# Optimization experiments

Measured on AMD Instinct MI355X. Metric: run time of the kernel, lower is better.

## Reference

```python
import jax, jax.numpy as jnp
import numpy as np

B, T, D = 4, 4096, 1024
EPS = 1e-5


def _layernorm(x, w):
    mu = jnp.mean(x, axis=-1, keepdims=True)
    var = jnp.var(x, axis=-1, keepdims=True)
    return (x - mu) * jax.lax.rsqrt(var + EPS) * w


def setup_inputs() -> dict:
    key = jax.random.key(0)
    k0, k1, k2, k3 = jax.random.split(key, 4)
    x = jax.random.normal(k0, (B, T, D), dtype=jnp.float32)
    lengths = jax.random.randint(k1, (B,), 1, T + 1, dtype=jnp.int32)
    ln1_w = jnp.ones((D,), dtype=jnp.float32)
    ln2_w = jnp.ones((D,), dtype=jnp.float32)
    Wfc = jax.random.normal(k2, (D, 4 * D), dtype=jnp.float32) * 0.02
    Wproj = jax.random.normal(k3, (4 * D, D), dtype=jnp.float32) * 0.02
    return {"x": x, "lengths": lengths, "ln1_w": ln1_w, "ln2_w": ln2_w,
            "Wfc": Wfc, "Wproj": Wproj}


def reference(x, lengths, ln1_w, ln2_w, Wfc, Wproj):
    b, t, d = x.shape
    # valid[b, i] = i < lengths[b]  (non-padded positions)
    valid = (jnp.arange(t)[None, :] < lengths[:, None]).astype(x.dtype)  # (B,T)

    # --- FusedQueryAtt: out[b,i] = h[b,i] + valid_i * sum_{j<=i} valid_j * gelu(h[b,j])
    h = _layernorm(x, ln1_w)
    g = jax.nn.gelu(h, approximate=False) * valid[:, :, None]  # (B,T,D)
    attn_out = h + valid[:, :, None] * jnp.cumsum(g, axis=1)
    x = x + attn_out  # residual around attn

    # --- MLP (bias=False, dropout=0 in eval)
    h2 = _layernorm(x, ln2_w)
    mlp_out = jax.nn.gelu(h2 @ Wfc, approximate=False) @ Wproj
    return x + mlp_out
```

## Files before the change

kernel.cpp:

```cpp
#include <hip/hip_runtime.h>
#include <hip/hip_bf16.h>
#include <math.h>

#define B_SZ 4
#define T_SZ 4096
#define D_SZ 1024
#define H_SZ 4096
#define CHUNK 16
#define NCHUNK (T_SZ / CHUNK)
#define NSEG 8
#define SEGC (NCHUNK / NSEG)
#define LN_EPS 1e-5f

using frag8 = __attribute__((ext_vector_type(8))) short;
using f32x4 = __attribute__((ext_vector_type(4))) float;

__device__ __forceinline__ float gelu_exact(float x) {
  return 0.5f * x * (1.0f + erff(x * 0.70710678118654752f));
}

__device__ __forceinline__ float gelu_fast(float x) {
  float u2 = 1.5957691216057308f * (x + 0.044715f * x * x * x);
  float e = __expf(u2);
  return x - x * __builtin_amdgcn_rcpf(e + 1.0f);
}

__device__ __forceinline__ unsigned short f2bf(float f) {
  unsigned u = __float_as_uint(f);
  u += 0x7fffu + ((u >> 16) & 1u);
  return (unsigned short)(u >> 16);
}

__global__ __launch_bounds__(256) void attn_phase1(
    const float* __restrict__ x, const int* __restrict__ lengths,
    const float* __restrict__ w1, float* __restrict__ partial,
    float* __restrict__ csum) {
  __shared__ float red[8];
  int b = blockIdx.x >> 8;
  int c = blockIdx.x & (NCHUNK - 1);
  int tid = threadIdx.x;
  int len = lengths[b];
  float4 w = ((const float4*)w1)[tid];
  float run0 = 0.f, run1 = 0.f, run2 = 0.f, run3 = 0.f;
  for (int i = 0; i < CHUNK; ++i) {
    int t = c * CHUNK + i;
    size_t row = ((size_t)b * T_SZ + t) * D_SZ;
    float4 v = ((const float4*)(x + row))[tid];
    float s = v.x + v.y + v.z + v.w;
    float q = v.x * v.x + v.y * v.y + v.z * v.z + v.w * v.w;
#pragma unroll
    for (int o = 32; o > 0; o >>= 1) {
      s += __shfl_xor(s, o, 64);
      q += __shfl_xor(q, o, 64);
    }
    if ((tid & 63) == 0) { red[(tid >> 6) * 2] = s; red[(tid >> 6) * 2 + 1] = q; }
    __syncthreads();
    s = red[0] + red[2] + red[4] + red[6];
    q = red[1] + red[3] + red[5] + red[7];
    __syncthreads();
    float mu = s * (1.0f / D_SZ);
    float var = q * (1.0f / D_SZ) - mu * mu;
    float rstd = rsqrtf(var + LN_EPS);
    bool valid = t < len;
    float hx = (v.x - mu) * rstd * w.x, hy = (v.y - mu) * rstd * w.y;
    float hz = (v.z - mu) * rstd * w.z, hw = (v.w - mu) * rstd * w.w;
    if (valid) {
      run0 += gelu_exact(hx); run1 += gelu_exact(hy);
      run2 += gelu_exact(hz); run3 += gelu_exact(hw);
    }
    float4 p;
    p.x = v.x + hx + (valid ? run0 : 0.f);
    p.y = v.y + hy + (valid ? run1 : 0.f);
    p.z = v.z + hz + (valid ? run2 : 0.f);
    p.w = v.w + hw + (valid ? run3 : 0.f);
    ((float4*)(partial + row))[tid] = p;
  }
  float4 cs; cs.x = run0; cs.y = run1; cs.z = run2; cs.w = run3;
  ((float4*)(csum + ((size_t)b * NCHUNK + c) * D_SZ))[tid] = cs;
}

__global__ __launch_bounds__(256) void seg_scan(float* __restrict__ csum,
                                                float* __restrict__ segsum) {
  int blk = blockIdx.x;
  int b = blk >> 5, seg = (blk >> 2) & 7, dq = blk & 3;
  int d = dq * 256 + threadIdx.x;
  float* p = csum + ((size_t)b * NCHUNK + seg * SEGC) * D_SZ + d;
  float acc = 0.f;
#pragma unroll 8
  for (int j = 0; j < SEGC; ++j) {
    float v = p[(size_t)j * D_SZ];
    p[(size_t)j * D_SZ] = acc;
    acc += v;
  }
  segsum[((size_t)b * NSEG + seg) * D_SZ + d] = acc;
}

__global__ __launch_bounds__(256) void seg_apply(
    float* __restrict__ csum, const float* __restrict__ segsum) {
  int blk = blockIdx.x;
  int b = blk >> 5, seg = (blk >> 2) & 7, dq = blk & 3;
  if (seg == 0) return;
  int d = dq * 256 + threadIdx.x;
  float off = 0.f;
  for (int s = 0; s < NSEG; ++s) {
    float v = segsum[((size_t)b * NSEG + s) * D_SZ + d];
    if (s < seg) off += v;
  }
  float* p = csum + ((size_t)b * NCHUNK + seg * SEGC) * D_SZ + d;
#pragma unroll 8
  for (int j = 0; j < SEGC; ++j) p[(size_t)j * D_SZ] += off;
}

__global__ __launch_bounds__(256) void attn_phase2_ln2(
    float* __restrict__ xres, const float* __restrict__ csum,
    const int* __restrict__ lengths, const float* __restrict__ w2,
    unsigned short* __restrict__ h2) {
  __shared__ float red[8];
  int t = blockIdx.x & (T_SZ - 1);
  int b = blockIdx.x >> 12;
  int tid = threadIdx.x;
  bool valid = t < lengths[b];
  int c = t / CHUNK;
  size_t row = ((size_t)b * T_SZ + t) * D_SZ;
  float4 v = ((const float4*)(xres + row))[tid];
  if (valid) {
    float4 o = ((const float4*)(csum + ((size_t)b * NCHUNK + c) * D_SZ))[tid];
    v.x += o.x; v.y += o.y; v.z += o.z; v.w += o.w;
  }
  ((float4*)(xres + row))[tid] = v;
  float s = v.x + v.y + v.z + v.w;
  float q = v.x * v.x + v.y * v.y + v.z * v.z + v.w * v.w;
#pragma unroll
  for (int o = 32; o > 0; o >>= 1) {
    s += __shfl_xor(s, o, 64);
    q += __shfl_xor(q, o, 64);
  }
  int wv = tid >> 6;
  if ((tid & 63) == 0) { red[wv * 2] = s; red[wv * 2 + 1] = q; }
  __syncthreads();
  s = red[0] + red[2] + red[4] + red[6];
  q = red[1] + red[3] + red[5] + red[7];
  float mu = s * (1.0f / D_SZ);
  float var = q * (1.0f / D_SZ) - mu * mu;
  float rstd = rsqrtf(var + LN_EPS);
  float4 w = ((const float4*)w2)[tid];
  ushort4 hq;
  hq.x = f2bf((v.x - mu) * rstd * w.x);
  hq.y = f2bf((v.y - mu) * rstd * w.y);
  hq.z = f2bf((v.z - mu) * rstd * w.z);
  hq.w = f2bf((v.w - mu) * rstd * w.w);
  ((ushort4*)(h2 + row))[tid] = hq;
}

__global__ __launch_bounds__(256) void transpose_f32_to_bf16(
    const float* __restrict__ src, unsigned short* __restrict__ dst,
    int R, int C) {
  __shared__ float tile[32][33];
  int bx = blockIdx.x * 32;
  int by = blockIdx.y * 32;
  int tx = threadIdx.x & 31;
  int ty = threadIdx.x >> 5;
#pragma unroll
  for (int i = 0; i < 32; i += 8)
    tile[ty + i][tx] = src[(size_t)(by + ty + i) * C + bx + tx];
  __syncthreads();
#pragma unroll
  for (int i = 0; i < 32; i += 8)
    dst[(size_t)(bx + ty + i) * R + by + tx] = f2bf(tile[tx][ty + i]);
}

#define GT_TILE (256 * 64)

#define GLD16(gsrc, ldsoff)                                                   \
  __builtin_amdgcn_global_load_lds(                                           \
      (const __attribute__((address_space(1))) unsigned int*)(gsrc),          \
      (__attribute__((address_space(3))) unsigned int*)(smc + (ldsoff)), 16,  \
      0, 0)

#define STAGE_A(h, DP, k0e)                                                   \
  do {                                                                        \
    GLD16(gA + (size_t)((h) * 64) * K + (k0e),                                \
          aW + (h) * 8192 + (DP) * 32768);                                    \
    GLD16(gA + (size_t)((h) * 64 + 128) * K + (k0e),                          \
          aW + (h) * 8192 + 16384 + (DP) * 32768);                            \
  } while (0)

#define STAGE_B(h, DP, k0e)                                                   \
  do {                                                                        \
    GLD16(gB + (size_t)((h) * 32) * K + (k0e),                                \
          bW + (h) * 4096 + (DP) * 32768);                                    \
    GLD16(gB + (size_t)((h) * 32 + 128) * K + (k0e),                          \
          bW + (h) * 4096 + 16384 + (DP) * 32768);                            \
  } while (0)

template <int CUR, int MH>
__device__ __forceinline__ void rd_af(const char* smc, int aB0, int aB1,
                                      frag8 (&af)[4][2]) {
#pragma unroll
  for (int tm = 0; tm < 4; ++tm) {
    af[tm][0] = *(const frag8*)(smc + aB0 + (CUR + MH * 8192 + tm * 2048));
    af[tm][1] = *(const frag8*)(smc + aB1 + (CUR + MH * 8192 + tm * 2048));
  }
}

template <int CUR, int NH>
__device__ __forceinline__ void rd_bf(const char* smc, int bB0, int bB1,
                                      frag8 (&bf)[2][2]) {
#pragma unroll
  for (int tn = 0; tn < 2; ++tn) {
    bf[tn][0] = *(const frag8*)(smc + bB0 + (CUR + NH * 4096 + tn * 2048));
    bf[tn][1] = *(const frag8*)(smc + bB1 + (CUR + NH * 4096 + tn * 2048));
  }
}

template <int MH, int NH>
__device__ __forceinline__ void mfma_q(f32x4 (&acc)[8][4],
                                       const frag8 (&a)[4][2],
                                       const frag8 (&b)[2][2]) {
#pragma unroll
  for (int kk = 0; kk < 2; ++kk)
#pragma unroll
    for (int tm = 0; tm < 4; ++tm)
#pragma unroll
      for (int tn = 0; tn < 2; ++tn)
        acc[MH * 4 + tm][NH * 2 + tn] =
            __builtin_amdgcn_mfma_f32_16x16x32_bf16(
                a[tm][kk], b[tn][kk], acc[MH * 4 + tm][NH * 2 + tn], 0, 0, 0);
}

#define GBAR()                          \
  do {                                  \
    asm volatile("" ::: "memory");      \
    __builtin_amdgcn_s_barrier();       \
    asm volatile("" ::: "memory");      \
  } while (0)

#define TILE_BODY(t, CURB, CURP, NXTB, NXTP)                                  \
  do {                                                                        \
    bool p1 = (t) + 1 < nt, p2 = (t) + 2 < nt;                                \
                     \
    rd_af<CURB, 0>(smc, aB0, aB1, af);                                        \
    if (p1) STAGE_A(1, NXTP, ((t) + 1) * 64);                                 \
    GBAR();                                                                   \
    __builtin_amdgcn_s_setprio(1);                                            \
    mfma_q<0, 0>(acc, af, b0);                                                \
    __builtin_amdgcn_s_setprio(0);                                            \
    GBAR();                                                                   \
           \
    rd_bf<CURB, 1>(smc, bB0, bB1, b1);                                        \
    if (p2) STAGE_A(0, CURP, ((t) + 2) * 64);                                 \
    GBAR();                                                                   \
    __builtin_amdgcn_s_setprio(1);                                            \
    mfma_q<0, 1>(acc, af, b1);                                                \
    __builtin_amdgcn_s_setprio(0);                                            \
    GBAR();                                                                   \
      \
    rd_af<CURB, 1>(smc, aB0, aB1, af);                                        \
    if (p2) STAGE_B(0, CURP, ((t) + 2) * 64);                                 \
    GBAR();                                                                   \
    __builtin_amdgcn_s_setprio(1);                                            \
    mfma_q<1, 1>(acc, af, b1);                                                \
    __builtin_amdgcn_s_setprio(0);                                            \
    GBAR();                                                                   \
                 \
    if (p2) {                                                                 \
      STAGE_B(1, CURP, ((t) + 2) * 64);                                       \
      asm volatile("s_waitcnt vmcnt(6)" ::: "memory");                        \
    } else {                                                                  \
      asm volatile("s_waitcnt vmcnt(0)" ::: "memory");                        \
    }                                                                         \
    GBAR();                                                                   \
    __builtin_amdgcn_s_setprio(1);                                            \
    mfma_q<1, 0>(acc, af, b0);                                                \
    __builtin_amdgcn_s_setprio(0);                                            \
    if (p1) rd_bf<NXTB, 0>(smc, bB0, bB1, b0);                                \
    GBAR();                                                                   \
  } while (0)

__global__ __launch_bounds__(512, 2) void gemm256_bt(
    const unsigned short* __restrict__ A, const unsigned short* __restrict__ Bt,
    int N, int K, int gx,
    const float* __restrict__ resid, float* __restrict__ outf,
    unsigned short* __restrict__ outb, int epi) {
  extern __shared__ char smc[];

  int orig = blockIdx.x, nwg = gridDim.x;
  int wg = orig;
  if ((nwg & 7) == 0) wg = (orig & 7) * (nwg >> 3) + (orig >> 3);
  int bx = wg % gx, by = wg / gx;
  int bm = by * 256, bn = bx * 256;

  int tid = threadIdx.x;
  int lane = tid & 63, wave = tid >> 6;
  int wm = wave >> 2, wn = wave & 3;
  int quad = lane >> 4, r16 = lane & 15;

  const unsigned short* A_blk = A + (size_t)bm * K;
  const unsigned short* B_blk = Bt + (size_t)bn * K;
  int nt = K >> 6;

  int swz = (r16 & 7) << 4;
  int aB0 = wm * 16384 + r16 * 128 + ((quad * 16) ^ swz);
  int aB1 = wm * 16384 + r16 * 128 + ((64 + quad * 16) ^ swz);
  int bB0 = 65536 + wn * 8192 + r16 * 128 + ((quad * 16) ^ swz);
  int bB1 = 65536 + wn * 8192 + r16 * 128 + ((64 + quad * 16) ^ swz);

  int arow = tid >> 3;
  int kc = ((tid & 7) * 8) ^ ((arow & 7) << 3);
  const unsigned short* gA = A_blk + (size_t)arow * K + kc;
  int browl = (arow >> 5) * 64 + (arow & 31);
  const unsigned short* gB = B_blk + (size_t)browl * K + kc;
  int aW = arow * 128 + (tid & 7) * 16;
  int bW = 65536 + browl * 128 + (tid & 7) * 16;

  f32x4 acc[8][4] = {};
  frag8 af[4][2];
  frag8 b0[2][2], b1[2][2];

  STAGE_A(0, 0, 0);
  STAGE_A(1, 0, 0);
  STAGE_B(0, 0, 0);
  STAGE_B(1, 0, 0);
  if (nt > 1) {
    STAGE_A(0, 1, 64);
    STAGE_B(0, 1, 64);
    STAGE_B(1, 1, 64);
    asm volatile("s_waitcnt vmcnt(6)" ::: "memory");
  } else {
    asm volatile("s_waitcnt vmcnt(0)" ::: "memory");
  }
  GBAR();
  rd_bf<0, 0>(smc, bB0, bB1, b0);

  for (int t = 0; t < nt; t += 2) {
    TILE_BODY(t, 0, 0, 32768, 1);
    TILE_BODY(t + 1, 32768, 1, 0, 0);
  }

  if (epi == 0) {
#pragma unroll
    for (int mf = 0; mf < 8; ++mf) {
#pragma unroll
      for (int nf = 0; nf < 4; ++nf) {
        int gm0 = bm + wm * 128 + mf * 16 + quad * 4;
        int gn = bn + wn * 64 + nf * 16 + r16;
#pragma unroll
        for (int r = 0; r < 4; ++r)
          outb[(size_t)(gm0 + r) * N + gn] = f2bf(gelu_fast(acc[mf][nf][r]));
      }
    }
  } else {
#pragma unroll
    for (int mf = 0; mf < 8; ++mf) {
#pragma unroll
      for (int nf = 0; nf < 4; ++nf) {
        int gm0 = bm + wm * 128 + mf * 16 + quad * 4;
        int gn = bn + wn * 64 + nf * 16 + r16;
#pragma unroll
        for (int r = 0; r < 4; ++r)
          outf[(size_t)(gm0 + r) * N + gn] =
              resid[(size_t)(gm0 + r) * N + gn] + acc[mf][nf][r];
      }
    }
  }
}

extern "C" void kernel_launch(void* const* d_in, const int* in_sizes, int n_in,
                              void* d_out, int out_size, void* d_ws,
                              size_t ws_size, hipStream_t stream) {
  const float* x = (const float*)d_in[0];
  const int* lengths = (const int*)d_in[1];
  const float* ln1_w = (const float*)d_in[2];
  const float* ln2_w = (const float*)d_in[3];
  const float* Wfc = (const float*)d_in[4];
  const float* Wproj = (const float*)d_in[5];
  float* out = (float*)d_out;

  static bool lds_cfg = false;
  if (!lds_cfg) {
    hipFuncSetAttribute((const void*)gemm256_bt,
                        hipFuncAttributeMaxDynamicSharedMemorySize, 131072);
    lds_cfg = true;
  }

  char* ws = (char*)d_ws;
  size_t off = 0;
  float* segsum = (float*)(ws + off);
  off += (size_t)B_SZ * NSEG * D_SZ * sizeof(float);
  float* csum = (float*)(ws + off);
  off += (size_t)B_SZ * NCHUNK * D_SZ * sizeof(float);
  unsigned short* wfcb = (unsigned short*)(ws + off);
  off += (size_t)D_SZ * H_SZ * sizeof(unsigned short);
  unsigned short* wprojb = (unsigned short*)(ws + off);
  off += (size_t)H_SZ * D_SZ * sizeof(unsigned short);
  unsigned short* h2 = (unsigned short*)(ws + off);
  off += (size_t)B_SZ * T_SZ * D_SZ * sizeof(unsigned short);
  unsigned short* act = (unsigned short*)(ws + off);

  const int M = B_SZ * T_SZ;
  const size_t tileBytes = 256ull * H_SZ * sizeof(unsigned short);
  size_t avail = (ws_size > off) ? (ws_size - off) : 0;
  int sliceTiles = (int)(avail / tileBytes);
  if (sliceTiles < 1) sliceTiles = 1;
  int sliceM = sliceTiles * 256;
  if (sliceM > M) sliceM = M;

  attn_phase1<<<B_SZ * NCHUNK, 256, 0, stream>>>(x, lengths, ln1_w, out, csum);
  seg_scan<<<B_SZ * NSEG * (D_SZ / 256), 256, 0, stream>>>(csum, segsum);
  seg_apply<<<B_SZ * NSEG * (D_SZ / 256), 256, 0, stream>>>(csum, segsum);
  attn_phase2_ln2<<<B_SZ * T_SZ, 256, 0, stream>>>(out, csum, lengths, ln2_w, h2);
  transpose_f32_to_bf16<<<dim3(H_SZ / 32, D_SZ / 32), 256, 0, stream>>>(
      Wfc, wfcb, D_SZ, H_SZ);
  transpose_f32_to_bf16<<<dim3(D_SZ / 32, H_SZ / 32), 256, 0, stream>>>(
      Wproj, wprojb, H_SZ, D_SZ);

  for (int m0 = 0; m0 < M; m0 += sliceM) {
    int rows = (M - m0 < sliceM) ? (M - m0) : sliceM;
    int r1 = rows / 256;
    gemm256_bt<<<dim3((H_SZ / 256) * r1), 512, 131072, stream>>>(
        h2 + (size_t)m0 * D_SZ, wfcb, H_SZ, D_SZ, H_SZ / 256,
        nullptr, nullptr, act, 0);
    gemm256_bt<<<dim3((D_SZ / 256) * r1), 512, 131072, stream>>>(
        act, wprojb, D_SZ, H_SZ, D_SZ / 256,
        out + (size_t)m0 * D_SZ, out + (size_t)m0 * D_SZ, nullptr, 1);
  }
}
```

Baseline: 458.4 us.

## Shrink GEMM tiles to 128x128 with simpler pipeline and fold seg_apply into phase2

Replaces the 256x256, 512-thread GEMM with a 128x128, 256-thread GEMM. The new kernel uses a simpler two-stage pipeline: one LDS read of the A and B fragments per K-tile, then 32 MFMAs, with the prefetch two tiles ahead. Separately, it drops the seg_apply kernel and has attn_phase2_ln2 add the preceding segment sums on the fly, which saves a launch and a read-modify-write pass over csum. The smaller tiles cut per-block LDS to allow more blocks and simpler scheduling. In exchange, data reuse per tile is lower, so global and LDS traffic go up, and the finely interleaved barrier schedule is lost.

```diff
diff --git a/kernel.cpp b/kernel.cpp
--- a/kernel.cpp
+++ b/kernel.cpp
@@ -95,36 +95,25 @@
   segsum[((size_t)b * NSEG + seg) * D_SZ + d] = acc;
 }
 
-__global__ __launch_bounds__(256) void seg_apply(
-    float* __restrict__ csum, const float* __restrict__ segsum) {
-  int blk = blockIdx.x;
-  int b = blk >> 5, seg = (blk >> 2) & 7, dq = blk & 3;
-  if (seg == 0) return;
-  int d = dq * 256 + threadIdx.x;
-  float off = 0.f;
-  for (int s = 0; s < NSEG; ++s) {
-    float v = segsum[((size_t)b * NSEG + s) * D_SZ + d];
-    if (s < seg) off += v;
-  }
-  float* p = csum + ((size_t)b * NCHUNK + seg * SEGC) * D_SZ + d;
-#pragma unroll 8
-  for (int j = 0; j < SEGC; ++j) p[(size_t)j * D_SZ] += off;
-}
-
 __global__ __launch_bounds__(256) void attn_phase2_ln2(
     float* __restrict__ xres, const float* __restrict__ csum,
-    const int* __restrict__ lengths, const float* __restrict__ w2,
-    unsigned short* __restrict__ h2) {
+    const float* __restrict__ segsum, const int* __restrict__ lengths,
+    const float* __restrict__ w2, unsigned short* __restrict__ h2) {
   __shared__ float red[8];
   int t = blockIdx.x & (T_SZ - 1);
   int b = blockIdx.x >> 12;
   int tid = threadIdx.x;
   bool valid = t < lengths[b];
   int c = t / CHUNK;
+  int seg = c >> 5;
   size_t row = ((size_t)b * T_SZ + t) * D_SZ;
   float4 v = ((const float4*)(xres + row))[tid];
   if (valid) {
     float4 o = ((const float4*)(csum + ((size_t)b * NCHUNK + c) * D_SZ))[tid];
+    for (int s = 0; s < seg; ++s) {
+      float4 g = ((const float4*)(segsum + ((size_t)b * NSEG + s) * D_SZ))[tid];
+      o.x += g.x; o.y += g.y; o.z += g.z; o.w += g.w;
+    }
     v.x += o.x; v.y += o.y; v.z += o.z; v.w += o.w;
   }
   ((float4*)(xres + row))[tid] = v;
@@ -169,63 +158,46 @@
     dst[(size_t)(bx + ty + i) * R + by + tx] = f2bf(tile[tx][ty + i]);
 }
 
-#define GT_TILE (256 * 64)
-
 #define GLD16(gsrc, ldsoff)                                                   \
   __builtin_amdgcn_global_load_lds(                                           \
       (const __attribute__((address_space(1))) unsigned int*)(gsrc),          \
       (__attribute__((address_space(3))) unsigned int*)(smc + (ldsoff)), 16,  \
       0, 0)
 
-#define STAGE_A(h, DP, k0e)                                                   \
+#define STAGE_A(P, k0e)                                                       \
   do {                                                                        \
-    GLD16(gA + (size_t)((h) * 64) * K + (k0e),                                \
-          aW + (h) * 8192 + (DP) * 32768);                                    \
-    GLD16(gA + (size_t)((h) * 64 + 128) * K + (k0e),                          \
-          aW + (h) * 8192 + 16384 + (DP) * 32768);                            \
+    GLD16(gA + (size_t)0 * K + (k0e), aW + 0 + (P));                          \
+    GLD16(gA + (size_t)32 * K + (k0e), aW + 4096 + (P));                      \
+    GLD16(gA + (size_t)64 * K + (k0e), aW + 8192 + (P));                      \
+    GLD16(gA + (size_t)96 * K + (k0e), aW + 12288 + (P));                     \
   } while (0)
 
-#define STAGE_B(h, DP, k0e)                                                   \
+#define STAGE_B(P, k0e)                                                       \
   do {                                                                        \
-    GLD16(gB + (size_t)((h) * 32) * K + (k0e),                                \
-          bW + (h) * 4096 + (DP) * 32768);                                    \
-    GLD16(gB + (size_t)((h) * 32 + 128) * K + (k0e),                          \
-          bW + (h) * 4096 + 16384 + (DP) * 32768);                            \
+    GLD16(gB + (size_t)0 * K + (k0e), bW + 0 + (P));                          \
+    GLD16(gB + (size_t)32 * K + (k0e), bW + 4096 + (P));                      \
+    GLD16(gB + (size_t)64 * K + (k0e), bW + 8192 + (P));                      \
+    GLD16(gB + (size_t)96 * K + (k0e), bW + 12288 + (P));                     \
   } while (0)
 
-template <int CUR, int MH>
+template <int P>
 __device__ __forceinline__ void rd_af(const char* smc, int aB0, int aB1,
                                       frag8 (&af)[4][2]) {
 #pragma unroll
   for (int tm = 0; tm < 4; ++tm) {
-    af[tm][0] = *(const frag8*)(smc + aB0 + (CUR + MH * 8192 + tm * 2048));
-    af[tm][1] = *(const frag8*)(smc + aB1 + (CUR + MH * 8192 + tm * 2048));
-  }
-}
-
-template <int CUR, int NH>
+    af[tm][0] = *(const frag8*)(smc + aB0 + (P + tm * 2048));
+    af[tm][1] = *(const frag8*)(smc + aB1 + (P + tm * 2048));
+  }
+}
+
+template <int P>
 __device__ __forceinline__ void rd_bf(const char* smc, int bB0, int bB1,
-                                      frag8 (&bf)[2][2]) {
-#pragma unroll
-  for (int tn = 0; tn < 2; ++tn) {
-    bf[tn][0] = *(const frag8*)(smc + bB0 + (CUR + NH * 4096 + tn * 2048));
-    bf[tn][1] = *(const frag8*)(smc + bB1 + (CUR + NH * 4096 + tn * 2048));
-  }
-}
-
-template <int MH, int NH>
-__device__ __forceinline__ void mfma_q(f32x4 (&acc)[8][4],
-                                       const frag8 (&a)[4][2],
-                                       const frag8 (&b)[2][2]) {
-#pragma unroll
-  for (int kk = 0; kk < 2; ++kk)
-#pragma unroll
-    for (int tm = 0; tm < 4; ++tm)
-#pragma unroll
-      for (int tn = 0; tn < 2; ++tn)
-        acc[MH * 4 + tm][NH * 2 + tn] =
-            __builtin_amdgcn_mfma_f32_16x16x32_bf16(
-                a[tm][kk], b[tn][kk], acc[MH * 4 + tm][NH * 2 + tn], 0, 0, 0);
+                                      frag8 (&bf)[4][2]) {
+#pragma unroll
+  for (int tn = 0; tn < 4; ++tn) {
+    bf[tn][0] = *(const frag8*)(smc + bB0 + (P + tn * 2048));
+    bf[tn][1] = *(const frag8*)(smc + bB1 + (P + tn * 2048));
+  }
 }
 
 #define GBAR()                          \
@@ -235,49 +207,32 @@
     asm volatile("" ::: "memory");      \
   } while (0)
 
-#define TILE_BODY(t, CURB, CURP, NXTB, NXTP)                                  \
+#define TILE_BODY(t, P)                                                       \
   do {                                                                        \
     bool p1 = (t) + 1 < nt, p2 = (t) + 2 < nt;                                \
-                     \
-    rd_af<CURB, 0>(smc, aB0, aB1, af);                                        \
-    if (p1) STAGE_A(1, NXTP, ((t) + 1) * 64);                                 \
+    rd_af<P>(smc, aB0, aB1, af);                                              \
+    rd_bf<P>(smc, bB0, bB1, bf);                                              \
+    asm volatile("s_waitcnt lgkmcnt(0)" ::: "memory");                        \
     GBAR();                                                                   \
+    if (p2) {                                                                 \
+      STAGE_A(P, ((t) + 2) * 64);                                             \
+      STAGE_B(P, ((t) + 2) * 64);                                             \
+    }                                                                         \
     __builtin_amdgcn_s_setprio(1);                                            \
-    mfma_q<0, 0>(acc, af, b0);                                                \
+    _Pragma("unroll") for (int kk = 0; kk < 2; ++kk)                          \
+        _Pragma("unroll") for (int tm = 0; tm < 4; ++tm)                      \
+            _Pragma("unroll") for (int tn = 0; tn < 4; ++tn)                  \
+                acc[tm][tn] = __builtin_amdgcn_mfma_f32_16x16x32_bf16(        \
+                    af[tm][kk], bf[tn][kk], acc[tm][tn], 0, 0, 0);            \
     __builtin_amdgcn_s_setprio(0);                                            \
-    GBAR();                                                                   \
-           \
-    rd_bf<CURB, 1>(smc, bB0, bB1, b1);                                        \
-    if (p2) STAGE_A(0, CURP, ((t) + 2) * 64);                                 \
-    GBAR();                                                                   \
-    __builtin_amdgcn_s_setprio(1);                                            \
-    mfma_q<0, 1>(acc, af, b1);                                                \
-    __builtin_amdgcn_s_setprio(0);                                            \
-    GBAR();                                                                   \
-      \
-    rd_af<CURB, 1>(smc, aB0, aB1, af);                                        \
-    if (p2) STAGE_B(0, CURP, ((t) + 2) * 64);                                 \
-    GBAR();                                                                   \
-    __builtin_amdgcn_s_setprio(1);                                            \
-    mfma_q<1, 1>(acc, af, b1);                                                \
-    __builtin_amdgcn_s_setprio(0);                                            \
-    GBAR();                                                                   \
-                 \
-    if (p2) {                                                                 \
-      STAGE_B(1, CURP, ((t) + 2) * 64);                                       \
-      asm volatile("s_waitcnt vmcnt(6)" ::: "memory");                        \
-    } else {                                                                  \
+    if (p2 && p1)                                                             \
+      asm volatile("s_waitcnt vmcnt(8)" ::: "memory");                        \
+    else                                                                      \
       asm volatile("s_waitcnt vmcnt(0)" ::: "memory");                        \
-    }                                                                         \
-    GBAR();                                                                   \
-    __builtin_amdgcn_s_setprio(1);                                            \
-    mfma_q<1, 0>(acc, af, b0);                                                \
-    __builtin_amdgcn_s_setprio(0);                                            \
-    if (p1) rd_bf<NXTB, 0>(smc, bB0, bB1, b0);                                \
     GBAR();                                                                   \
   } while (0)
 
-__global__ __launch_bounds__(512, 2) void gemm256_bt(
+__global__ __launch_bounds__(256, 2) void gemm128_bt(
     const unsigned short* __restrict__ A, const unsigned short* __restrict__ Bt,
     int N, int K, int gx,
     const float* __restrict__ resid, float* __restrict__ outf,
@@ -288,11 +243,11 @@
   int wg = orig;
   if ((nwg & 7) == 0) wg = (orig & 7) * (nwg >> 3) + (orig >> 3);
   int bx = wg % gx, by = wg / gx;
-  int bm = by * 256, bn = bx * 256;
+  int bm = by * 128, bn = bx * 128;
 
   int tid = threadIdx.x;
   int lane = tid & 63, wave = tid >> 6;
-  int wm = wave >> 2, wn = wave & 3;
+  int wm = wave >> 1, wn = wave & 1;
   int quad = lane >> 4, r16 = lane & 15;
 
   const unsigned short* A_blk = A + (size_t)bm * K;
@@ -300,66 +255,60 @@
   int nt = K >> 6;
 
   int swz = (r16 & 7) << 4;
-  int aB0 = wm * 16384 + r16 * 128 + ((quad * 16) ^ swz);
-  int aB1 = wm * 16384 + r16 * 128 + ((64 + quad * 16) ^ swz);
-  int bB0 = 65536 + wn * 8192 + r16 * 128 + ((quad * 16) ^ swz);
-  int bB1 = 65536 + wn * 8192 + r16 * 128 + ((64 + quad * 16) ^ swz);
+  int aB0 = (wm * 64 + r16) * 128 + ((quad * 16) ^ swz);
+  int aB1 = (wm * 64 + r16) * 128 + ((64 + quad * 16) ^ swz);
+  int bB0 = 32768 + (wn * 64 + r16) * 128 + ((quad * 16) ^ swz);
+  int bB1 = 32768 + (wn * 64 + r16) * 128 + ((64 + quad * 16) ^ swz);
 
   int arow = tid >> 3;
   int kc = ((tid & 7) * 8) ^ ((arow & 7) << 3);
   const unsigned short* gA = A_blk + (size_t)arow * K + kc;
-  int browl = (arow >> 5) * 64 + (arow & 31);
-  const unsigned short* gB = B_blk + (size_t)browl * K + kc;
+  const unsigned short* gB = B_blk + (size_t)arow * K + kc;
   int aW = arow * 128 + (tid & 7) * 16;
-  int bW = 65536 + browl * 128 + (tid & 7) * 16;
-
-  f32x4 acc[8][4] = {};
-  frag8 af[4][2];
-  frag8 b0[2][2], b1[2][2];
-
-  STAGE_A(0, 0, 0);
-  STAGE_A(1, 0, 0);
-  STAGE_B(0, 0, 0);
-  STAGE_B(1, 0, 0);
+  int bW = 32768 + arow * 128 + (tid & 7) * 16;
+
+  f32x4 acc[4][4] = {};
+  frag8 af[4][2], bf[4][2];
+
+  STAGE_A(0, 0);
+  STAGE_B(0, 0);
   if (nt > 1) {
-    STAGE_A(0, 1, 64);
-    STAGE_B(0, 1, 64);
-    STAGE_B(1, 1, 64);
-    asm volatile("s_waitcnt vmcnt(6)" ::: "memory");
+    STAGE_A(16384, 64);
+    STAGE_B(16384, 64);
+    asm volatile("s_waitcnt vmcnt(8)" ::: "memory");
   } else {
     asm volatile("s_waitcnt vmcnt(0)" ::: "memory");
   }
   GBAR();
-  rd_bf<0, 0>(smc, bB0, bB1, b0);
 
   for (int t = 0; t < nt; t += 2) {
-    TILE_BODY(t, 0, 0, 32768, 1);
-    TILE_BODY(t + 1, 32768, 1, 0, 0);
+    TILE_BODY(t, 0);
+    TILE_BODY(t + 1, 16384);
   }
 
   if (epi == 0) {
 #pragma unroll
-    for (int mf = 0; mf < 8; ++mf) {
-#pragma unroll
-      for (int nf = 0; nf < 4; ++nf) {
-        int gm0 = bm + wm * 128 + mf * 16 + quad * 4;
-        int gn = bn + wn * 64 + nf * 16 + r16;
+    for (int tm = 0; tm < 4; ++tm) {
+#pragma unroll
+      for (int tn = 0; tn < 4; ++tn) {
+        int gm0 = bm + wm * 64 + tm * 16 + quad * 4;
+        int gn = bn + wn * 64 + tn * 16 + r16;
 #pragma unroll
         for (int r = 0; r < 4; ++r)
-          outb[(size_t)(gm0 + r) * N + gn] = f2bf(gelu_fast(acc[mf][nf][r]));
+          outb[(size_t)(gm0 + r) * N + gn] = f2bf(gelu_fast(acc[tm][tn][r]));
       }
     }
   } else {
 #pragma unroll
-    for (int mf = 0; mf < 8; ++mf) {
-#pragma unroll
-      for (int nf = 0; nf < 4; ++nf) {
-        int gm0 = bm + wm * 128 + mf * 16 + quad * 4;
-        int gn = bn + wn * 64 + nf * 16 + r16;
+    for (int tm = 0; tm < 4; ++tm) {
+#pragma unroll
+      for (int tn = 0; tn < 4; ++tn) {
+        int gm0 = bm + wm * 64 + tm * 16 + quad * 4;
+        int gn = bn + wn * 64 + tn * 16 + r16;
 #pragma unroll
         for (int r = 0; r < 4; ++r)
           outf[(size_t)(gm0 + r) * N + gn] =
-              resid[(size_t)(gm0 + r) * N + gn] + acc[mf][nf][r];
+              resid[(size_t)(gm0 + r) * N + gn] + acc[tm][tn][r];
       }
     }
   }
@@ -378,8 +327,8 @@
 
   static bool lds_cfg = false;
   if (!lds_cfg) {
-    hipFuncSetAttribute((const void*)gemm256_bt,
-                        hipFuncAttributeMaxDynamicSharedMemorySize, 131072);
+    hipFuncSetAttribute((const void*)gemm128_bt,
+                        hipFuncAttributeMaxDynamicSharedMemorySize, 65536);
     lds_cfg = true;
   }
 
@@ -407,8 +356,8 @@
 
   attn_phase1<<<B_SZ * NCHUNK, 256, 0, stream>>>(x, lengths, ln1_w, out, csum);
   seg_scan<<<B_SZ * NSEG * (D_SZ / 256), 256, 0, stream>>>(csum, segsum);
-  seg_apply<<<B_SZ * NSEG * (D_SZ / 256), 256, 0, stream>>>(csum, segsum);
-  attn_phase2_ln2<<<B_SZ * T_SZ, 256, 0, stream>>>(out, csum, lengths, ln2_w, h2);
+  attn_phase2_ln2<<<B_SZ * T_SZ, 256, 0, stream>>>(out, csum, segsum, lengths,
+                                                   ln2_w, h2);
   transpose_f32_to_bf16<<<dim3(H_SZ / 32, D_SZ / 32), 256, 0, stream>>>(
       Wfc, wfcb, D_SZ, H_SZ);
   transpose_f32_to_bf16<<<dim3(D_SZ / 32, H_SZ / 32), 256, 0, stream>>>(
@@ -416,12 +365,12 @@
 
   for (int m0 = 0; m0 < M; m0 += sliceM) {
     int rows = (M - m0 < sliceM) ? (M - m0) : sliceM;
-    int r1 = rows / 256;
-    gemm256_bt<<<dim3((H_SZ / 256) * r1), 512, 131072, stream>>>(
-        h2 + (size_t)m0 * D_SZ, wfcb, H_SZ, D_SZ, H_SZ / 256,
+    int rb = rows / 128;
+    gemm128_bt<<<dim3((H_SZ / 128) * rb), 256, 65536, stream>>>(
+        h2 + (size_t)m0 * D_SZ, wfcb, H_SZ, D_SZ, H_SZ / 128,
         nullptr, nullptr, act, 0);
-    gemm256_bt<<<dim3((D_SZ / 256) * r1), 512, 131072, stream>>>(
-        act, wprojb, D_SZ, H_SZ, D_SZ / 256,
+    gemm128_bt<<<dim3((D_SZ / 128) * rb), 256, 65536, stream>>>(
+        act, wprojb, D_SZ, H_SZ, D_SZ / 128,
         out + (size_t)m0 * D_SZ, out + (size_t)m0 * D_SZ, nullptr, 1);
   }
 }
```

New measurement: 481.5 us. +5.0%, slower.
